# Performance work log

Hardware: AMD Instinct MI355X
Metric: run time of the kernel (lower is better)

## Reference

```python
import jax, jax.numpy as jnp
import numpy as np

MAX_DEG = 3
DEG_DIMS = [1, 3, 5, 7]          # degree_to_dim(d) = 2d+1
SUM_DIM = 16                     # sum of DEG_DIMS
FREQ_SUM = 44                    # sum over (d_in,d_out) of 2*min(d_in,d_out)+1
C = 32                           # channels per degree (in == out, FULL fusion)
EDGE_DIM = 2                     # fiber_edge[0] + 1
MID = 32                         # RadialProfile mid_dim
E = 4096
N = 1024


def setup_inputs() -> dict:
    key = jax.random.key(0)
    ks = jax.random.split(key, 16)
    inp = {}
    for d, dim in enumerate(DEG_DIMS):
        inp[f"node_feats_{d}"] = jax.random.normal(ks[d], (N, C, dim), jnp.float32)
    inp["edge_feats_0"] = jax.random.normal(ks[4], (E, EDGE_DIM, 1), jnp.float32)
    inp["basis"] = jax.random.normal(ks[5], (E, SUM_DIM, FREQ_SUM, SUM_DIM), jnp.float32)
    inp["src"] = jax.random.randint(ks[6], (E,), 0, N, dtype=jnp.int32)
    inp["dst"] = jax.random.randint(ks[7], (E,), 0, N, dtype=jnp.int32)
    # RadialProfile params: Linear(2,32) -> ReLU -> Linear(32,32) -> ReLU -> Linear(32, 44*32*32, bias=False)
    inp["w1"] = jax.random.normal(ks[8], (EDGE_DIM, MID), jnp.float32) / np.sqrt(EDGE_DIM)
    inp["b1"] = jnp.zeros((MID,), jnp.float32)
    inp["w2"] = jax.random.normal(ks[9], (MID, MID), jnp.float32) / np.sqrt(MID)
    inp["b2"] = jnp.zeros((MID,), jnp.float32)
    inp["w3"] = jax.random.normal(ks[10], (MID, FREQ_SUM * C * C), jnp.float32) / np.sqrt(MID)
    # self-interaction kernels per output degree
    for d in range(MAX_DEG + 1):
        inp[f"kernel_self_{d}"] = jax.random.normal(ks[11 + d], (C, C), jnp.float32) / np.sqrt(C)
    return inp


def _conv_se3(node_feats, edge_feats_0, basis, src, dst,
              w1, b1, w2, b2, w3, kernels_self):
    e = edge_feats_0.shape[0]
    # invariant edge feats: [E, edge_dim]
    inv = edge_feats_0[..., 0]
    # gather source node features and fuse along representation dim: [E, C, 16]
    feats = jnp.concatenate([nf[src] for nf in node_feats], axis=-1)
    # RadialProfile MLP -> radial weights [E, C_out, C_in * FREQ_SUM]
    h = jax.nn.relu(inv @ w1 + b1)
    h = jax.nn.relu(h @ w2 + b2)
    radial_weights = (h @ w3).reshape(e, C, C * FREQ_SUM)
    # VersatileConvSE3 fused path:
    # tmp = (features @ basis_view).view(E, C*FREQ_SUM, SUM_DIM)
    basis_view = basis.reshape(e, SUM_DIM, FREQ_SUM * SUM_DIM)
    tmp = jnp.einsum('eci,eix->ecx', feats, basis_view).reshape(e, C * FREQ_SUM, SUM_DIM)
    out_fused = jnp.einsum('eok,eks->eos', radial_weights, tmp)  # [E, C, 16]
    # unfuse by degree, add self-interaction at dst, pool (copy_e_sum) to nodes
    outs = []
    off = 0
    for d, dim in enumerate(DEG_DIMS):
        o = out_fused[..., off:off + dim]
        o = o + jnp.einsum('oc,ecd->eod', kernels_self[d], node_feats[d][dst])
        outs.append(jax.ops.segment_sum(o, dst, num_segments=N))
        off += dim
    # return fused node output [N, C, 16] (concat of degrees 0..3)
    return jnp.concatenate(outs, axis=-1)


def reference(node_feats_0, node_feats_1, node_feats_2, node_feats_3,
              edge_feats_0, basis, src, dst,
              w1, b1, w2, b2, w3,
              kernel_self_0, kernel_self_1, kernel_self_2, kernel_self_3):
    return _conv_se3([node_feats_0, node_feats_1, node_feats_2, node_feats_3],
                     edge_feats_0, basis, src, dst,
                     w1, b1, w2, b2, w3,
                     [kernel_self_0, kernel_self_1, kernel_self_2, kernel_self_3])
```

## Files before the change

kernel.cpp:

```cpp
#include <hip/hip_runtime.h>
#include <hip/hip_bf16.h>

#define NN 1024
#define EE 4096
#define CC 32
#define SD 16
#define FQ 44
#define MIDC 32
#define EB 16
#define NFQ 4
#define FPB 11

typedef short s16x4 __attribute__((ext_vector_type(4)));
typedef short s16x8 __attribute__((ext_vector_type(8)));
typedef float fx4 __attribute__((ext_vector_type(4)));

__device__ __forceinline__ unsigned short f2b(float x) {
    __hip_bfloat16 b = __float2bfloat16(x);
    return *reinterpret_cast<unsigned short*>(&b);
}

__device__ __forceinline__ s16x4 pack4(float a, float b, float c, float d) {
    s16x4 r;
    r[0] = (short)f2b(a); r[1] = (short)f2b(b);
    r[2] = (short)f2b(c); r[3] = (short)f2b(d);
    return r;
}

__device__ __forceinline__ fx4 mfma16(s16x4 a, s16x4 b, fx4 c) {
#if defined(__HIP_DEVICE_COMPILE__)
#if __has_builtin(__builtin_amdgcn_mfma_f32_16x16x16_bf16)
    return __builtin_amdgcn_mfma_f32_16x16x16_bf16(a, b, c, 0, 0, 0);
#else
    return __builtin_amdgcn_mfma_f32_16x16x16bf16_1k(a, b, c, 0, 0, 0);
#endif
#else
    return c;
#endif
}

#define CBAR() asm volatile("s_waitcnt lgkmcnt(0)\n\ts_barrier" ::: "memory")

__global__ __launch_bounds__(256) void k_w3t2(const float* __restrict__ w3,
                                              unsigned short* __restrict__ w3t2) {
    int tid = blockIdx.x * 256 + threadIdx.x;
    int m = tid & 31;
    int o = (tid >> 5) & 31;
    int c = tid >> 10;
    const float* rp = &w3[(size_t)m * 45056 + o * 1408 + c * 44];
    float v[44];
#pragma unroll
    for (int q = 0; q < 11; q++) {
        float4 t4 = *(const float4*)(rp + q * 4);
        v[q * 4 + 0] = t4.x; v[q * 4 + 1] = t4.y;
        v[q * 4 + 2] = t4.z; v[q * 4 + 3] = t4.w;
    }
#pragma unroll
    for (int f = 0; f < FQ; f++) {
        w3t2[(((size_t)f * CC + o) * CC + c) * CC + m] = f2b(v[f]);
    }
}

__global__ __launch_bounds__(256) void k_h(const float* __restrict__ ef,
                                           const float* __restrict__ w1,
                                           const float* __restrict__ b1,
                                           const float* __restrict__ w2,
                                           const float* __restrict__ b2,
                                           const int* __restrict__ dst,
                                           unsigned short* __restrict__ h2,
                                           int* __restrict__ deg) {
    int e = blockIdx.x * 256 + threadIdx.x;
    if (e >= EE) return;
    float i0 = ef[e * 2 + 0], i1 = ef[e * 2 + 1];
    float h1[MIDC];
#pragma unroll
    for (int j = 0; j < MIDC; j++) {
        float v = i0 * w1[j] + i1 * w1[MIDC + j] + b1[j];
        h1[j] = v > 0.f ? v : 0.f;
    }
    for (int j = 0; j < MIDC; j++) {
        float v = b2[j];
#pragma unroll
        for (int m = 0; m < MIDC; m++) v += h1[m] * w2[m * MIDC + j];
        v = v > 0.f ? v : 0.f;
        h2[e * MIDC + j] = f2b(v);
    }
    atomicAdd(&deg[dst[e]], 1);
}

__global__ __launch_bounds__(512, 4) void k_main(
    const float* __restrict__ nf0, const float* __restrict__ nf1,
    const float* __restrict__ nf2, const float* __restrict__ nf3,
    const float* __restrict__ basis, const int* __restrict__ src,
    const int* __restrict__ dst, const unsigned short* __restrict__ h2,
    const unsigned short* __restrict__ w3t2, float* __restrict__ out) {
    __shared__ __align__(16) unsigned short rad_lds[2][EB * CC * CC];

    int t = threadIdx.x;
    int wv = t >> 6;
    int l = t & 63;
    int l15 = l & 15;
    int kg = l >> 4;
    int fq = blockIdx.x >> 8;
    int eg = blockIdx.x & 255;
    int eb = eg * EB;
    int f0 = fq * FPB;

    s16x8 h2frag = *(const s16x8*)(h2 + ((size_t)(eb + l15) * MIDC + (kg << 3)));

    s16x4 fa[2][2];
#pragma unroll
    for (int ei = 0; ei < 2; ei++) {
        int sn = src[eb + (wv << 1) + ei];
#pragma unroll
        for (int ch = 0; ch < 2; ch++) {
            int c = (ch << 4) + l15;
            s16x4 v;
#pragma unroll
            for (int j = 0; j < 4; j++) {
                int i = (kg << 2) + j;
                float x;
                if (i < 1) x = nf0[sn * CC + c];
                else if (i < 4) x = nf1[(sn * CC + c) * 3 + (i - 1)];
                else if (i < 9) x = nf2[(sn * CC + c) * 5 + (i - 4)];
                else x = nf3[(sn * CC + c) * 7 + (i - 9)];
                v[j] = (short)f2b(x);
            }
            fa[ei][ch] = v;
        }
    }

    int radw[8];
#pragma unroll
    for (int j = 0; j < 8; j++) {
        int o = (wv << 2) + (j >> 1), ch = j & 1;
        int b = (l15 << 11) | (o << 6) | (ch << 5) | (kg << 3);
        radw[j] = b ^ (((l15 ^ o) & 15) << 3);
    }
    int rada[2][2][2];
#pragma unroll
    for (int ei = 0; ei < 2; ei++) {
        int e = (wv << 1) + ei;
#pragma unroll
        for (int oh = 0; oh < 2; oh++) {
            int o = (oh << 4) + l15;
#pragma unroll
            for (int ch = 0; ch < 2; ch++) {
                int b = (e << 11) | (o << 6) | (ch << 5) | (kg << 3);
                rada[ei][oh][ch] = b ^ (((e ^ o) & 15) << 3);
            }
        }
    }

    fx4 acc[2][2];
#pragma unroll
    for (int q = 0; q < 4; q++) acc[q >> 1][q & 1] = (fx4){0.f, 0.f, 0.f, 0.f};
    fx4 zz = (fx4){0.f, 0.f, 0.f, 0.f};

    s16x8 w[8];
    float pfA[2][4], pfB[2][4];

#define LOAD_W(F)                                                                       \
    {                                                                                   \
        _Pragma("unroll") for (int j = 0; j < 8; j++) {                                 \
            int o_ = (wv << 2) + (j >> 1), ch_ = j & 1;                                 \
            w[j] = *(const s16x8*)(w3t2 +                                               \
                ((((size_t)(F) * CC + o_) * CC + (ch_ << 4) + l15) * CC + (kg << 3)));  \
        }                                                                               \
    }
#define LOAD_PF(F, SLOT)                                                                \
    {                                                                                   \
        _Pragma("unroll") for (int ei_ = 0; ei_ < 2; ei_++) {                           \
            const float* bp = basis +                                                   \
                (((size_t)(eb + (wv << 1) + ei_) * SD + (kg << 2)) * FQ + (F)) * SD +   \
                l15;                                                                    \
            _Pragma("unroll") for (int j = 0; j < 4; j++)                               \
                SLOT[ei_][j] = bp[(size_t)j * (FQ * SD)];                               \
        }                                                                               \
    }
#define RAD(BUF)                                                                        \
    {                                                                                   \
        __builtin_amdgcn_s_setprio(1);                                                  \
        _Pragma("unroll") for (int j = 0; j < 8; j++) {                                 \
            fx4 cf = __builtin_amdgcn_mfma_f32_16x16x32_bf16(w[j], h2frag, zz, 0, 0, 0);\
            *(s16x4*)((char*)rad_lds[BUF] + radw[j]) = pack4(cf[0], cf[1], cf[2], cf[3]);\
        }                                                                               \
        __builtin_amdgcn_s_setprio(0);                                                  \
    }

    LOAD_PF(f0, pfA);
    LOAD_W(f0);
    LOAD_PF(f0 + 1, pfB);
    RAD(0);
    LOAD_W(f0 + 1);
    CBAR();

#pragma unroll
    for (int fi = 0; fi < FPB; fi++) {
        int f = f0 + fi;
        int cur = fi & 1;
        s16x4 bbf[2];
        if (cur == 0) {
            bbf[0] = pack4(pfA[0][0], pfA[0][1], pfA[0][2], pfA[0][3]);
            bbf[1] = pack4(pfA[1][0], pfA[1][1], pfA[1][2], pfA[1][3]);
        } else {
            bbf[0] = pack4(pfB[0][0], pfB[0][1], pfB[0][2], pfB[0][3]);
            bbf[1] = pack4(pfB[1][0], pfB[1][1], pfB[1][2], pfB[1][3]);
        }
        if (fi + 2 < FPB) {
            if (cur == 0) { LOAD_PF(f + 2, pfA); }
            else          { LOAD_PF(f + 2, pfB); }
        }
        if (fi + 1 < FPB) RAD(cur ^ 1);
        if (fi + 2 < FPB) LOAD_W(f + 2);

        __builtin_amdgcn_s_setprio(1);
#pragma unroll
        for (int ei = 0; ei < 2; ei++) {
#pragma unroll
            for (int ch = 0; ch < 2; ch++) {
                fx4 u = mfma16(fa[ei][ch], bbf[ei], zz);
                s16x4 ub = pack4(u[0], u[1], u[2], u[3]);
#pragma unroll
                for (int oh = 0; oh < 2; oh++) {
                    s16x4 ra = *(const s16x4*)((char*)rad_lds[cur] + rada[ei][oh][ch]);
                    acc[ei][oh] = mfma16(ra, ub, acc[ei][oh]);
                }
            }
        }
        __builtin_amdgcn_s_setprio(0);
        if (fi + 1 < FPB) CBAR();
    }

#pragma unroll
    for (int ei = 0; ei < 2; ei++) {
        int e = (wv << 1) + ei;
        int d = dst[eb + e];
        float* op = &out[(size_t)d * (CC * SD)];
#pragma unroll
        for (int oh = 0; oh < 2; oh++) {
#pragma unroll
            for (int r = 0; r < 4; r++) {
                int o = (oh << 4) + (kg << 2) + r;
                atomicAdd(&op[o * SD + l15], acc[ei][oh][r]);
            }
        }
    }
}

__global__ __launch_bounds__(256) void k_self(
    const float* __restrict__ nf0, const float* __restrict__ nf1,
    const float* __restrict__ nf2, const float* __restrict__ nf3,
    const float* __restrict__ ks0, const float* __restrict__ ks1,
    const float* __restrict__ ks2, const float* __restrict__ ks3,
    const int* __restrict__ deg, float* __restrict__ out) {
    int idx = blockIdx.x * 256 + threadIdx.x;
    if (idx >= NN * CC * SD) return;
    int n = idx >> 9;
    int rem = idx & 511;
    int o = rem >> 4;
    int s = rem & 15;
    const float* nf;
    const float* ks;
    int dim, off;
    if (s < 1) { nf = nf0; ks = ks0; dim = 1; off = 0; }
    else if (s < 4) { nf = nf1; ks = ks1; dim = 3; off = 1; }
    else if (s < 9) { nf = nf2; ks = ks2; dim = 5; off = 4; }
    else { nf = nf3; ks = ks3; dim = 7; off = 9; }
    int j = s - off;
    float acc = 0.f;
#pragma unroll
    for (int c = 0; c < CC; c++) acc += ks[o * CC + c] * nf[(n * CC + c) * dim + j];
    out[idx] += (float)deg[n] * acc;
}

extern "C" void kernel_launch(void* const* d_in, const int* in_sizes, int n_in,
                              void* d_out, int out_size, void* d_ws, size_t ws_size,
                              hipStream_t stream) {
    const float* nf0 = (const float*)d_in[0];
    const float* nf1 = (const float*)d_in[1];
    const float* nf2 = (const float*)d_in[2];
    const float* nf3 = (const float*)d_in[3];
    const float* ef = (const float*)d_in[4];
    const float* basis = (const float*)d_in[5];
    const int* src = (const int*)d_in[6];
    const int* dst = (const int*)d_in[7];
    const float* w1 = (const float*)d_in[8];
    const float* b1 = (const float*)d_in[9];
    const float* w2 = (const float*)d_in[10];
    const float* b2 = (const float*)d_in[11];
    const float* w3 = (const float*)d_in[12];
    const float* ks0 = (const float*)d_in[13];
    const float* ks1 = (const float*)d_in[14];
    const float* ks2 = (const float*)d_in[15];
    const float* ks3 = (const float*)d_in[16];
    float* out = (float*)d_out;

    unsigned short* h2 = (unsigned short*)d_ws;
    int* deg = (int*)((char*)d_ws + EE * MIDC * 2);
    unsigned short* w3t2 = (unsigned short*)((char*)d_ws + EE * MIDC * 2 + 4096);

    (void)hipMemsetAsync(d_out, 0, (size_t)out_size * sizeof(float), stream);
    (void)hipMemsetAsync(deg, 0, NN * sizeof(int), stream);

    k_w3t2<<<128, 256, 0, stream>>>(w3, w3t2);
    k_h<<<EE / 256, 256, 0, stream>>>(ef, w1, b1, w2, b2, dst, h2, deg);
    k_main<<<(EE / EB) * NFQ, 512, 0, stream>>>(nf0, nf1, nf2, nf3, basis, src, dst,
                                                h2, w3t2, out);
    k_self<<<(NN * CC * SD) / 256, 256, 0, stream>>>(nf0, nf1, nf2, nf3, ks0, ks1,
                                                     ks2, ks3, deg, out);
}
```

Baseline: 120.4 us.

## Stage basis through LDS with coalesced float4 loads and drop frequency-split grid

Each block now processes all 44 frequencies for its 16 edges instead of splitting frequencies across four blocks. Basis slices of four frequencies are loaded with coalesced float4 reads, converted to bf16 and written transposed into a double-buffered LDS staging area. The MFMA loop then reads operands from LDS. This removes the strided scalar basis gathers and the four-way atomic output contention, at the cost of a quarter as many blocks (256), more LDS per block and lower occupancy.

```diff
diff --git a/kernel.cpp b/kernel.cpp
--- a/kernel.cpp
+++ b/kernel.cpp
@@ -8,8 +8,8 @@
 #define FQ 44
 #define MIDC 32
 #define EB 16
-#define NFQ 4
-#define FPB 11
+#define NCH 11
+#define CF 4
 
 typedef short s16x4 __attribute__((ext_vector_type(4)));
 typedef short s16x8 __attribute__((ext_vector_type(8)));
@@ -24,6 +24,15 @@
     s16x4 r;
     r[0] = (short)f2b(a); r[1] = (short)f2b(b);
     r[2] = (short)f2b(c); r[3] = (short)f2b(d);
+    return r;
+}
+
+__device__ __forceinline__ s16x8 pack8(float4 a, float4 b) {
+    s16x8 r;
+    r[0] = (short)f2b(a.x); r[1] = (short)f2b(a.y);
+    r[2] = (short)f2b(a.z); r[3] = (short)f2b(a.w);
+    r[4] = (short)f2b(b.x); r[5] = (short)f2b(b.y);
+    r[6] = (short)f2b(b.z); r[7] = (short)f2b(b.w);
     return r;
 }
 
@@ -88,23 +97,21 @@
     atomicAdd(&deg[dst[e]], 1);
 }
 
-__global__ __launch_bounds__(512, 4) void k_main(
+__global__ __launch_bounds__(512, 2) void k_main(
     const float* __restrict__ nf0, const float* __restrict__ nf1,
     const float* __restrict__ nf2, const float* __restrict__ nf3,
     const float* __restrict__ basis, const int* __restrict__ src,
     const int* __restrict__ dst, const unsigned short* __restrict__ h2,
     const unsigned short* __restrict__ w3t2, float* __restrict__ out) {
     __shared__ __align__(16) unsigned short rad_lds[2][EB * CC * CC];
+    __shared__ __align__(16) unsigned short basT[2][EB * CF * SD * SD];
 
     int t = threadIdx.x;
     int wv = t >> 6;
     int l = t & 63;
     int l15 = l & 15;
     int kg = l >> 4;
-    int fq = blockIdx.x >> 8;
-    int eg = blockIdx.x & 255;
-    int eb = eg * EB;
-    int f0 = fq * FPB;
+    int eb = blockIdx.x * EB;
 
     s16x8 h2frag = *(const s16x8*)(h2 + ((size_t)(eb + l15) * MIDC + (kg << 3)));
 
@@ -157,9 +164,31 @@
     for (int q = 0; q < 4; q++) acc[q >> 1][q & 1] = (fx4){0.f, 0.f, 0.f, 0.f};
     fx4 zz = (fx4){0.f, 0.f, 0.f, 0.f};
 
+    int e_s = t >> 5;
+    int i_s = t & 15;
+    int fp = (t >> 4) & 1;
+    const float* sbase =
+        basis + ((size_t)(eb + e_s) * SD + i_s) * (FQ * SD) + fp * (2 * SD);
+    int row = ((i_s & 3) << 2) | (i_s >> 2);
+    int stg_dst = (e_s << 10) | (fp << 9) | (row << 4);
+
+    float4 sreg[8];
+#define LOAD_STG(CH)                                                                    \
+    {                                                                                   \
+        const float4* p = (const float4*)(sbase + (CH) * (CF * SD));                    \
+        _Pragma("unroll") for (int q = 0; q < 8; q++) sreg[q] = p[q];                   \
+        asm volatile("" ::: "memory");                                                  \
+    }
+#define WRITE_STG(H)                                                                    \
+    {                                                                                   \
+        _Pragma("unroll") for (int f2 = 0; f2 < 2; f2++)                                \
+        _Pragma("unroll") for (int sh = 0; sh < 2; sh++) {                              \
+            s16x8 v = pack8(sreg[f2 * 4 + sh * 2], sreg[f2 * 4 + sh * 2 + 1]);          \
+            *(s16x8*)(&basT[H][stg_dst + (f2 << 8) + (sh << 3)]) = v;                   \
+        }                                                                               \
+    }
+
     s16x8 w[8];
-    float pfA[2][4], pfB[2][4];
-
 #define LOAD_W(F)                                                                       \
     {                                                                                   \
         _Pragma("unroll") for (int j = 0; j < 8; j++) {                                 \
@@ -167,16 +196,7 @@
             w[j] = *(const s16x8*)(w3t2 +                                               \
                 ((((size_t)(F) * CC + o_) * CC + (ch_ << 4) + l15) * CC + (kg << 3)));  \
         }                                                                               \
-    }
-#define LOAD_PF(F, SLOT)                                                                \
-    {                                                                                   \
-        _Pragma("unroll") for (int ei_ = 0; ei_ < 2; ei_++) {                           \
-            const float* bp = basis +                                                   \
-                (((size_t)(eb + (wv << 1) + ei_) * SD + (kg << 2)) * FQ + (F)) * SD +   \
-                l15;                                                                    \
-            _Pragma("unroll") for (int j = 0; j < 4; j++)                               \
-                SLOT[ei_][j] = bp[(size_t)j * (FQ * SD)];                               \
-        }                                                                               \
+        asm volatile("" ::: "memory");                                                  \
     }
 #define RAD(BUF)                                                                        \
     {                                                                                   \
@@ -188,48 +208,58 @@
         __builtin_amdgcn_s_setprio(0);                                                  \
     }
 
-    LOAD_PF(f0, pfA);
-    LOAD_W(f0);
-    LOAD_PF(f0 + 1, pfB);
+    LOAD_STG(0);
+    WRITE_STG(0);
+    LOAD_STG(1);
+    LOAD_W(0);
     RAD(0);
-    LOAD_W(f0 + 1);
+    LOAD_W(1);
     CBAR();
 
-#pragma unroll
-    for (int fi = 0; fi < FPB; fi++) {
-        int f = f0 + fi;
-        int cur = fi & 1;
-        s16x4 bbf[2];
-        if (cur == 0) {
-            bbf[0] = pack4(pfA[0][0], pfA[0][1], pfA[0][2], pfA[0][3]);
-            bbf[1] = pack4(pfA[1][0], pfA[1][1], pfA[1][2], pfA[1][3]);
-        } else {
-            bbf[0] = pack4(pfB[0][0], pfB[0][1], pfB[0][2], pfB[0][3]);
-            bbf[1] = pack4(pfB[1][0], pfB[1][1], pfB[1][2], pfB[1][3]);
-        }
-        if (fi + 2 < FPB) {
-            if (cur == 0) { LOAD_PF(f + 2, pfA); }
-            else          { LOAD_PF(f + 2, pfB); }
-        }
-        if (fi + 1 < FPB) RAD(cur ^ 1);
-        if (fi + 2 < FPB) LOAD_W(f + 2);
-
-        __builtin_amdgcn_s_setprio(1);
-#pragma unroll
-        for (int ei = 0; ei < 2; ei++) {
-#pragma unroll
-            for (int ch = 0; ch < 2; ch++) {
-                fx4 u = mfma16(fa[ei][ch], bbf[ei], zz);
-                s16x4 ub = pack4(u[0], u[1], u[2], u[3]);
-#pragma unroll
-                for (int oh = 0; oh < 2; oh++) {
-                    s16x4 ra = *(const s16x4*)((char*)rad_lds[cur] + rada[ei][oh][ch]);
-                    acc[ei][oh] = mfma16(ra, ub, acc[ei][oh]);
+    for (int ch = 0; ch < NCH; ++ch) {
+        int h = ch & 1;
+        if (ch + 1 < NCH) {
+            WRITE_STG((ch + 1) & 1);
+            if (ch + 2 < NCH) LOAD_STG(ch + 2);
+        }
+        const unsigned short* btc = &basT[h][0];
+#pragma unroll
+        for (int k = 0; k < CF; ++k) {
+            int f = (ch << 2) + k;
+            int cur = k & 1;
+            s16x4 bbf[2];
+#pragma unroll
+            for (int ei = 0; ei < 2; ei++) {
+                const unsigned short* bb =
+                    btc + (((wv << 1) + ei) << 10) + (k << 8) + (kg << 4) + l15;
+                s16x4 v;
+                v[0] = (short)bb[0];
+                v[1] = (short)bb[64];
+                v[2] = (short)bb[128];
+                v[3] = (short)bb[192];
+                bbf[ei] = v;
+            }
+            if (f + 1 < FQ) RAD(cur ^ 1);
+            if (f + 2 < FQ) LOAD_W(f + 2);
+
+            __builtin_amdgcn_s_setprio(1);
+#pragma unroll
+            for (int ei = 0; ei < 2; ei++) {
+#pragma unroll
+                for (int ch_c = 0; ch_c < 2; ch_c++) {
+                    fx4 u = mfma16(fa[ei][ch_c], bbf[ei], zz);
+                    s16x4 ub = pack4(u[0], u[1], u[2], u[3]);
+#pragma unroll
+                    for (int oh = 0; oh < 2; oh++) {
+                        s16x4 ra =
+                            *(const s16x4*)((char*)rad_lds[cur] + rada[ei][oh][ch_c]);
+                        acc[ei][oh] = mfma16(ra, ub, acc[ei][oh]);
+                    }
                 }
             }
-        }
-        __builtin_amdgcn_s_setprio(0);
-        if (fi + 1 < FPB) CBAR();
+            __builtin_amdgcn_s_setprio(0);
+            if (f + 1 < FQ) CBAR();
+        }
     }
 
 #pragma unroll
@@ -305,8 +335,8 @@
 
     k_w3t2<<<128, 256, 0, stream>>>(w3, w3t2);
     k_h<<<EE / 256, 256, 0, stream>>>(ef, w1, b1, w2, b2, dst, h2, deg);
-    k_main<<<(EE / EB) * NFQ, 512, 0, stream>>>(nf0, nf1, nf2, nf3, basis, src, dst,
-                                                h2, w3t2, out);
+    k_main<<<EE / EB, 512, 0, stream>>>(nf0, nf1, nf2, nf3, basis, src, dst,
+                                        h2, w3t2, out);
     k_self<<<(NN * CC * SD) / 256, 256, 0, stream>>>(nf0, nf1, nf2, nf3, ks0, ks1,
                                                      ks2, ks3, deg, out);
 }
```

New measurement: 122.4 us. No clear change (+1.6%).

## Single-buffer radial LDS tile and restructure per-frequency pipeline with two barriers

Applied to the files above, without the earlier changes.

Replaces the double-buffered radial-weight LDS tile with a single buffer. Each frequency iteration now computes its radial weights, writes them to LDS, barriers, consumes them, then barriers again. The w3 prefetch depth drops from two frequencies ahead to one, compiler memory fences are added after the loads, and the s_setprio hints are removed. Halving the LDS footprint may let more blocks fit per CU, at the cost of an extra barrier per iteration and less overlap between radial-weight production and consumption.

```diff
diff --git a/kernel.cpp b/kernel.cpp
--- a/kernel.cpp
+++ b/kernel.cpp
@@ -40,6 +40,7 @@
 }
 
 #define CBAR() asm volatile("s_waitcnt lgkmcnt(0)\n\ts_barrier" ::: "memory")
+#define MEMFENCE() asm volatile("" ::: "memory")
 
 __global__ __launch_bounds__(256) void k_w3t2(const float* __restrict__ w3,
                                               unsigned short* __restrict__ w3t2) {
@@ -94,7 +95,7 @@
     const float* __restrict__ basis, const int* __restrict__ src,
     const int* __restrict__ dst, const unsigned short* __restrict__ h2,
     const unsigned short* __restrict__ w3t2, float* __restrict__ out) {
-    __shared__ __align__(16) unsigned short rad_lds[2][EB * CC * CC];
+    __shared__ __align__(16) unsigned short rad_lds[EB * CC * CC];
 
     int t = threadIdx.x;
     int wv = t >> 6;
@@ -167,6 +168,7 @@
             w[j] = *(const s16x8*)(w3t2 +                                               \
                 ((((size_t)(F) * CC + o_) * CC + (ch_ << 4) + l15) * CC + (kg << 3)));  \
         }                                                                               \
+        MEMFENCE();                                                                     \
     }
 #define LOAD_PF(F, SLOT)                                                                \
     {                                                                                   \
@@ -177,44 +179,35 @@
             _Pragma("unroll") for (int j = 0; j < 4; j++)                               \
                 SLOT[ei_][j] = bp[(size_t)j * (FQ * SD)];                               \
         }                                                                               \
-    }
-#define RAD(BUF)                                                                        \
-    {                                                                                   \
-        __builtin_amdgcn_s_setprio(1);                                                  \
-        _Pragma("unroll") for (int j = 0; j < 8; j++) {                                 \
-            fx4 cf = __builtin_amdgcn_mfma_f32_16x16x32_bf16(w[j], h2frag, zz, 0, 0, 0);\
-            *(s16x4*)((char*)rad_lds[BUF] + radw[j]) = pack4(cf[0], cf[1], cf[2], cf[3]);\
-        }                                                                               \
-        __builtin_amdgcn_s_setprio(0);                                                  \
+        MEMFENCE();                                                                     \
     }
 
     LOAD_PF(f0, pfA);
     LOAD_W(f0);
     LOAD_PF(f0 + 1, pfB);
-    RAD(0);
-    LOAD_W(f0 + 1);
-    CBAR();
 
 #pragma unroll
     for (int fi = 0; fi < FPB; fi++) {
         int f = f0 + fi;
-        int cur = fi & 1;
+#pragma unroll
+        for (int j = 0; j < 8; j++) {
+            fx4 cf = __builtin_amdgcn_mfma_f32_16x16x32_bf16(w[j], h2frag, zz, 0, 0, 0);
+            *(s16x4*)((char*)rad_lds + radw[j]) = pack4(cf[0], cf[1], cf[2], cf[3]);
+        }
+        if (fi + 1 < FPB) LOAD_W(f + 1);
+
         s16x4 bbf[2];
-        if (cur == 0) {
+        if ((fi & 1) == 0) {
             bbf[0] = pack4(pfA[0][0], pfA[0][1], pfA[0][2], pfA[0][3]);
             bbf[1] = pack4(pfA[1][0], pfA[1][1], pfA[1][2], pfA[1][3]);
+            if (fi + 2 < FPB) { LOAD_PF(f + 2, pfA); }
         } else {
             bbf[0] = pack4(pfB[0][0], pfB[0][1], pfB[0][2], pfB[0][3]);
             bbf[1] = pack4(pfB[1][0], pfB[1][1], pfB[1][2], pfB[1][3]);
-        }
-        if (fi + 2 < FPB) {
-            if (cur == 0) { LOAD_PF(f + 2, pfA); }
-            else          { LOAD_PF(f + 2, pfB); }
-        }
-        if (fi + 1 < FPB) RAD(cur ^ 1);
-        if (fi + 2 < FPB) LOAD_W(f + 2);
-
-        __builtin_amdgcn_s_setprio(1);
+            if (fi + 2 < FPB) { LOAD_PF(f + 2, pfB); }
+        }
+        CBAR();
+
 #pragma unroll
         for (int ei = 0; ei < 2; ei++) {
 #pragma unroll
@@ -223,12 +216,11 @@
                 s16x4 ub = pack4(u[0], u[1], u[2], u[3]);
 #pragma unroll
                 for (int oh = 0; oh < 2; oh++) {
-                    s16x4 ra = *(const s16x4*)((char*)rad_lds[cur] + rada[ei][oh][ch]);
+                    s16x4 ra = *(const s16x4*)((char*)rad_lds + rada[ei][oh][ch]);
                     acc[ei][oh] = mfma16(ra, ub, acc[ei][oh]);
                 }
             }
         }
-        __builtin_amdgcn_s_setprio(0);
         if (fi + 1 < FPB) CBAR();
     }
 
```

New measurement: 126.6 us. 5.2% more time.
